# Kernel optimization log

Measured on AMD Instinct MI355X. Metric: run time of the kernel, lower is better.

## Reference

```python
import jax, jax.numpy as jnp
import numpy as np

N_NODES = 100000
N_EDGES = 3200000
N_GRAPHS = 256
IN_DIM = 128
HID = 64
K = 3


def setup_inputs() -> dict:
    key = jax.random.key(0)
    ks = jax.random.split(key, 10)
    x = jax.random.normal(ks[0], (N_NODES, IN_DIM), dtype=jnp.float32)
    edge_index = jax.random.randint(ks[1], (2, N_EDGES), 0, N_NODES, dtype=jnp.int64)
    batch = jnp.sort(jax.random.randint(ks[2], (N_NODES,), 0, N_GRAPHS, dtype=jnp.int64))
    # ChebConv k-order weights: list of Linear(in, out) -> stacked [K, in, out]
    s1 = 1.0 / np.sqrt(IN_DIM)
    s2 = 1.0 / np.sqrt(HID)
    W1 = jax.random.uniform(ks[3], (K, IN_DIM, HID), jnp.float32, -s1, s1)
    b1 = jax.random.uniform(ks[4], (HID,), jnp.float32, -s1, s1)
    W2 = jax.random.uniform(ks[5], (K, HID, HID), jnp.float32, -s2, s2)
    b2 = jax.random.uniform(ks[6], (HID,), jnp.float32, -s2, s2)
    Wfc = jax.random.uniform(ks[7], (HID, 1), jnp.float32, -s2, s2)
    bfc = jax.random.uniform(ks[8], (1,), jnp.float32, -s2, s2)
    return {"x": x, "edge_index": edge_index, "batch": batch,
            "W1": W1, "b1": b1, "W2": W2, "b2": b2, "Wfc": Wfc, "bfc": bfc}


def _cheb_conv(x, src, dst, edge_w, W, b):
    # PyG ChebConv, sym normalization, lambda_max=2 => L_hat has zero diagonal
    # and off-diagonal -D^{-1/2} A D^{-1/2} (edge_w precomputed, negative).
    n = x.shape[0]
    def lhat(v):  # (L_hat v)_i = sum_{edges j->i} edge_w * v_j
        return jax.ops.segment_sum(edge_w[:, None] * v[src], dst, num_segments=n)
    Tx0 = x
    Tx1 = lhat(Tx0)
    Tx2 = 2.0 * lhat(Tx1) - Tx0
    return Tx0 @ W[0] + Tx1 @ W[1] + Tx2 @ W[2] + b


def reference(x, edge_index, batch, W1, b1, W2, b2, Wfc, bfc):
    src, dst = edge_index[0], edge_index[1]
    n = x.shape[0]
    # degree on row (source), sym normalization
    deg = jax.ops.segment_sum(jnp.ones_like(src, dtype=x.dtype), src, num_segments=n)
    dinv = jnp.where(deg > 0, jax.lax.rsqrt(jnp.maximum(deg, 1.0)), 0.0)
    edge_w = -dinv[src] * dinv[dst]  # scaled Laplacian off-diagonal weights

    h = jax.nn.relu(_cheb_conv(x, src, dst, edge_w, W1, b1))
    h = jax.nn.relu(_cheb_conv(h, src, dst, edge_w, W2, b2))

    # global mean pool over graphs
    sums = jax.ops.segment_sum(h, batch, num_segments=N_GRAPHS)
    counts = jax.ops.segment_sum(jnp.ones((n,), dtype=h.dtype), batch, num_segments=N_GRAPHS)
    pooled = sums / jnp.maximum(counts, 1.0)[:, None]

    return (pooled @ Wfc + bfc).squeeze(-1)  # [N_GRAPHS]
```

## Files before the change

### kernel.cpp

```cpp
#include <hip/hip_runtime.h>
#include <hip/hip_fp16.h>
#include <cstdint>
#include <cstddef>

static constexpr int NN = 100000;
static constexpr int NE = 3200000;
static constexpr int NG = 256;
static constexpr int NBK = (NN + 127) / 128;
static constexpr int EPB = NE / 256;

typedef _Float16 h8 __attribute__((ext_vector_type(8)));
typedef float f4v __attribute__((ext_vector_type(4)));

__device__ __forceinline__ void atomAddF(float* p, float v) {
  unsafeAtomicAdd(p, v);
}

__device__ __forceinline__ float h2f(__half h) { return __half2float(h); }

__device__ __forceinline__ unsigned pk2(float a, float b) {
  unsigned lo = __half_as_ushort(__float2half_rn(a));
  unsigned hi = __half_as_ushort(__float2half_rn(b));
  return lo | (hi << 16);
}

__global__ void k_detect(const int* __restrict__ ei, int* __restrict__ flag) {
  if (threadIdx.x == 0 && blockIdx.x == 0) {
    int nz = 0;
    for (int i = 0; i < 64; ++i) nz += (ei[2 * i + 1] != 0) ? 1 : 0;
    *flag = (nz == 0) ? 1 : 0;
  }
}

__device__ __forceinline__ int ld_idx(const void* raw, int f, int i) {
  return f ? (int)((const long long*)raw)[i] : ((const int*)raw)[i];
}

__global__ __launch_bounds__(256) void k_repack_batch(const void* __restrict__ raw,
                                                      const int* __restrict__ flag,
                                                      int* __restrict__ b32,
                                                      int* __restrict__ gcnt) {
  __shared__ int cnt[256];
  int t = threadIdx.x;
  cnt[t] = 0;
  int blk0 = blockIdx.x * 256;
  int f = *flag;
  int g0 = ld_idx(raw, f, blk0);
  __syncthreads();
  int i = blk0 + t;
  if (i < NN) {
    int g = ld_idx(raw, f, i);
    b32[i] = g;
    atomicAdd(&cnt[g - g0], 1);
  }
  __syncthreads();
  if (cnt[t] > 0) atomicAdd(&gcnt[g0 + t], cnt[t]);
}

__global__ __launch_bounds__(256) void k_hist(const void* __restrict__ raw,
                                              const int* __restrict__ flag,
                                              int* __restrict__ sCnt,
                                              int* __restrict__ dCnt,
                                              int* __restrict__ hsBlk,
                                              int* __restrict__ hdBlk) {
  __shared__ int hs[NBK], hd[NBK];
  int t = threadIdx.x;
  for (int i = t; i < NBK; i += 256) { hs[i] = 0; hd[i] = 0; }
  __syncthreads();
  int f = *flag;
  int e0 = blockIdx.x * EPB;
  for (int e = e0 + t; e < e0 + EPB; e += 256) {
    int s = ld_idx(raw, f, e);
    int d = ld_idx(raw, f, NE + e);
    atomicAdd(&hs[s >> 7], 1);
    atomicAdd(&hd[d >> 7], 1);
  }
  __syncthreads();
  size_t hb = (size_t)blockIdx.x * NBK;
  for (int i = t; i < NBK; i += 256) {
    int a = hs[i], b = hd[i];
    hsBlk[hb + i] = a;
    hdBlk[hb + i] = b;
    if (a) atomicAdd(&sCnt[i], a);
    if (b) atomicAdd(&dCnt[i], b);
  }
}

__global__ __launch_bounds__(1024) void k_scan(const int* __restrict__ sCnt,
                                               const int* __restrict__ dCnt,
                                               int* __restrict__ sBase,
                                               int* __restrict__ dBase,
                                               int* __restrict__ sCur,
                                               int* __restrict__ dCur) {
  __shared__ int sh1[1024], sh2[1024];
  int t = threadIdx.x;
  int v1 = (t < NBK) ? sCnt[t] : 0;
  int v2 = (t < NBK) ? dCnt[t] : 0;
  sh1[t] = v1; sh2[t] = v2;
  __syncthreads();
  for (int off = 1; off < 1024; off <<= 1) {
    int a1 = (t >= off) ? sh1[t - off] : 0;
    int a2 = (t >= off) ? sh2[t - off] : 0;
    __syncthreads();
    sh1[t] += a1; sh2[t] += a2;
    __syncthreads();
  }
  if (t <= NBK) {
    int b1 = sh1[t] - v1, b2 = sh2[t] - v2;
    sBase[t] = b1; dBase[t] = b2;
    if (t < NBK) { sCur[t] = b1; dCur[t] = b2; }
  }
}

__global__ __launch_bounds__(256) void k_scatter(const void* __restrict__ raw,
                                                 const int* __restrict__ flag,
                                                 const int* __restrict__ hsBlk,
                                                 const int* __restrict__ hdBlk,
                                                 int* __restrict__ sCur,
                                                 int* __restrict__ dCur,
                                                 int* __restrict__ srclist,
                                                 unsigned* __restrict__ elist) {
  __shared__ int hs[NBK], hd[NBK], cbS[NBK], cbD[NBK];
  int t = threadIdx.x;
  size_t hb = (size_t)blockIdx.x * NBK;
  for (int i = t; i < NBK; i += 256) {
    int c1 = hsBlk[hb + i];
    cbS[i] = c1 ? atomicAdd(&sCur[i], c1) : 0;
    int c2 = hdBlk[hb + i];
    cbD[i] = c2 ? atomicAdd(&dCur[i], c2) : 0;
    hs[i] = 0; hd[i] = 0;
  }
  __syncthreads();
  int f = *flag;
  int e0 = blockIdx.x * EPB;
  for (int e = e0 + t; e < e0 + EPB; e += 256) {
    int s = ld_idx(raw, f, e);
    int d = ld_idx(raw, f, NE + e);
    int bs = s >> 7, bd = d >> 7;
    int ls = atomicAdd(&hs[bs], 1);
    int ld2 = atomicAdd(&hd[bd], 1);
    srclist[cbS[bs] + ls] = s;
    elist[cbD[bd] + ld2] = (unsigned)s | ((unsigned)(d & 127) << 17);
  }
}

__global__ __launch_bounds__(256) void k_deg(const int* __restrict__ sBase,
                                             const int* __restrict__ srclist,
                                             float* __restrict__ dinv) {
  __shared__ int cnt[128];
  int t = threadIdx.x;
  if (t < 128) cnt[t] = 0;
  __syncthreads();
  int b = blockIdx.x;
  int e0 = sBase[b], e1 = sBase[b + 1];
  for (int i = e0 + t; i < e1; i += 256) atomicAdd(&cnt[srclist[i] & 127], 1);
  __syncthreads();
  if (t < 128) {
    int node = b * 128 + t;
    if (node < NN) {
      int c = cnt[t];
      dinv[node] = (c > 0) ? rsqrtf((float)c) : 0.f;
    }
  }
}

__global__ __launch_bounds__(256) void k_csr(const int* __restrict__ dBase,
                                             const unsigned* __restrict__ elist,
                                             int* __restrict__ rowptr,
                                             int* __restrict__ adj) {
  __shared__ int cnt[128], sc[128], off[128], fill[128];
  int t = threadIdx.x;
  if (t < 128) { cnt[t] = 0; fill[t] = 0; }
  __syncthreads();
  int b = blockIdx.x;
  int e0 = dBase[b], e1 = dBase[b + 1];
  for (int i = e0 + t; i < e1; i += 256) atomicAdd(&cnt[elist[i] >> 17], 1);
  __syncthreads();
  if (t < 128) sc[t] = cnt[t];
  __syncthreads();
  for (int o = 1; o < 128; o <<= 1) {
    int a = (t < 128 && t >= o) ? sc[t - o] : 0;
    __syncthreads();
    if (t < 128) sc[t] += a;
    __syncthreads();
  }
  if (t < 128) {
    off[t] = sc[t] - cnt[t];
    int node = b * 128 + t;
    if (node < NN) rowptr[node] = e0 + off[t];
  }
  if (b == NBK - 1 && t == 0) rowptr[NN] = e1;
  __syncthreads();
  for (int i = e0 + t; i < e1; i += 256) {
    unsigned w2 = elist[i];
    int l = (int)(w2 >> 17);
    int pos = atomicAdd(&fill[l], 1);
    adj[e0 + off[l] + pos] = (int)(w2 & 0x1FFFFu);
  }
}

__global__ __launch_bounds__(256) void k_prepW(const float* __restrict__ W1,
                                               const float* __restrict__ W2,
                                               __half* __restrict__ BtX,
                                               __half* __restrict__ BtH) {
  int t = blockIdx.x * 256 + threadIdx.x;
  if (t < 192 * 128) {
    int n = t >> 7, k = t & 127;
    float v;
    if (n < 64)       v = W1[k * 64 + n] - W1[16384 + k * 64 + n];
    else if (n < 128) v = W1[8192 + k * 64 + (n - 64)];
    else              v = W1[16384 + k * 64 + (n - 128)];
    BtX[n * 128 + k] = __float2half_rn(v);
  } else if (t < 192 * 128 + 64 * 192) {
    int u = t - 192 * 128;
    int n = u / 192, k = u % 192;
    int s = k >> 6, kk = k & 63;
    float v = (s == 0) ? (W2[kk * 64 + n] - W2[8192 + kk * 64 + n])
            : (s == 1) ? W2[4096 + kk * 64 + n]
                       : 2.f * W2[8192 + kk * 64 + n];
    BtH[n * 192 + k] = __float2half_rn(v);
  }
}

static constexpr int AW = 136;
__global__ __launch_bounds__(256) void k_gemm_x(const float* __restrict__ x,
                                                const __half* __restrict__ BtX,
                                                const float* __restrict__ dinv,
                                                __half* __restrict__ gV0,
                                                unsigned* __restrict__ p01) {
  __shared__ __align__(16) _Float16 As[128 * AW];
  const int t = threadIdx.x;
  const int n0 = blockIdx.x * 128;
  {
    int i = t >> 1, q = t & 1;
    int row = n0 + i;
    _Float16* dst = As + i * AW + q * 64;
    if (row < NN) {
      const float* src = x + (size_t)row * 128 + q * 64;
#pragma unroll
      for (int c = 0; c < 64; c += 4) {
        float4 v = *reinterpret_cast<const float4*>(src + c);
        ushort4 u;
        u.x = __half_as_ushort(__float2half_rn(v.x));
        u.y = __half_as_ushort(__float2half_rn(v.y));
        u.z = __half_as_ushort(__float2half_rn(v.z));
        u.w = __half_as_ushort(__float2half_rn(v.w));
        *reinterpret_cast<ushort4*>(dst + c) = u;
      }
    } else {
#pragma unroll
      for (int c = 0; c < 64; c += 4)
        *reinterpret_cast<ushort4*>(dst + c) = make_ushort4(0, 0, 0, 0);
    }
  }
  __syncthreads();
  const int w = t >> 6, lane = t & 63;
  const int quad = lane >> 4, l = lane & 15;
  f4v acc[2][12];
#pragma unroll
  for (int mt = 0; mt < 2; ++mt)
#pragma unroll
    for (int nt = 0; nt < 12; ++nt) acc[mt][nt] = (f4v){0.f, 0.f, 0.f, 0.f};

#pragma unroll
  for (int ks = 0; ks < 4; ++ks) {
    int k0 = ks * 32 + quad * 8;
    h8 a0 = *reinterpret_cast<const h8*>(As + (w * 32 + l) * AW + k0);
    h8 a1 = *reinterpret_cast<const h8*>(As + (w * 32 + 16 + l) * AW + k0);
#pragma unroll
    for (int nt = 0; nt < 12; ++nt) {
      h8 b = *reinterpret_cast<const h8*>(BtX + (size_t)(nt * 16 + l) * 128 + k0);
      acc[0][nt] = __builtin_amdgcn_mfma_f32_16x16x32_f16(a0, b, acc[0][nt], 0, 0, 0);
      acc[1][nt] = __builtin_amdgcn_mfma_f32_16x16x32_f16(a1, b, acc[1][nt], 0, 0, 0);
    }
  }
#pragma unroll
  for (int mt = 0; mt < 2; ++mt) {
#pragma unroll
    for (int r = 0; r < 4; ++r) {
      int row = n0 + w * 32 + mt * 16 + quad * 4 + r;
      if (row < NN) {
        float dv = dinv[row];
#pragma unroll
        for (int nt2 = 0; nt2 < 4; ++nt2) {
          gV0[(size_t)row * 64 + nt2 * 16 + l] = __float2half_rn(acc[mt][nt2][r]);
          p01[(size_t)row * 64 + nt2 * 16 + l] =
              pk2(dv * acc[mt][4 + nt2][r], dv * acc[mt][8 + nt2][r]);
        }
      }
    }
  }
}

__global__ __launch_bounds__(256) void k_prop2p(const int* __restrict__ rp,
                                                const int* __restrict__ adj,
                                                const unsigned* __restrict__ vp,
                                                const float* __restrict__ dinv,
                                                __half* __restrict__ oA,
                                                __half* __restrict__ oB) {
  int node = blockIdx.x * 4 + (threadIdx.x >> 6);
  int d = threadIdx.x & 63;
  if (node >= NN) return;
  int p0 = rp[node], p1 = rp[node + 1];
  float a0 = 0.f, a1 = 0.f, a2 = 0.f, a3 = 0.f;
  float b0 = 0.f, b1 = 0.f, b2 = 0.f, b3 = 0.f;
  union { unsigned u; __half2 h; } cv;
  int p = p0;
  int pA = (p0 + 3) & ~3;
  if (pA > p1) pA = p1;
  for (; p < pA; ++p) {
    cv.u = vp[(size_t)adj[p] * 64 + d];
    float2 f = __half22float2(cv.h);
    a0 += f.x; b0 += f.y;
  }
  for (; p + 8 <= p1; p += 8) {
    int4 e0 = *reinterpret_cast<const int4*>(adj + p);
    int4 e1 = *reinterpret_cast<const int4*>(adj + p + 4);
    unsigned u0 = vp[(size_t)e0.x * 64 + d], u1 = vp[(size_t)e0.y * 64 + d];
    unsigned u2 = vp[(size_t)e0.z * 64 + d], u3 = vp[(size_t)e0.w * 64 + d];
    unsigned u4 = vp[(size_t)e1.x * 64 + d], u5 = vp[(size_t)e1.y * 64 + d];
    unsigned u6 = vp[(size_t)e1.z * 64 + d], u7 = vp[(size_t)e1.w * 64 + d];
    cv.u = u0; { float2 f = __half22float2(cv.h); a0 += f.x; b0 += f.y; }
    cv.u = u1; { float2 f = __half22float2(cv.h); a1 += f.x; b1 += f.y; }
    cv.u = u2; { float2 f = __half22float2(cv.h); a2 += f.x; b2 += f.y; }
    cv.u = u3; { float2 f = __half22float2(cv.h); a3 += f.x; b3 += f.y; }
    cv.u = u4; { float2 f = __half22float2(cv.h); a0 += f.x; b0 += f.y; }
    cv.u = u5; { float2 f = __half22float2(cv.h); a1 += f.x; b1 += f.y; }
    cv.u = u6; { float2 f = __half22float2(cv.h); a2 += f.x; b2 += f.y; }
    cv.u = u7; { float2 f = __half22float2(cv.h); a3 += f.x; b3 += f.y; }
  }
  if (p + 4 <= p1) {
    int4 e = *reinterpret_cast<const int4*>(adj + p);
    unsigned u0 = vp[(size_t)e.x * 64 + d], u1 = vp[(size_t)e.y * 64 + d];
    unsigned u2 = vp[(size_t)e.z * 64 + d], u3 = vp[(size_t)e.w * 64 + d];
    cv.u = u0; { float2 f = __half22float2(cv.h); a0 += f.x; b0 += f.y; }
    cv.u = u1; { float2 f = __half22float2(cv.h); a1 += f.x; b1 += f.y; }
    cv.u = u2; { float2 f = __half22float2(cv.h); a2 += f.x; b2 += f.y; }
    cv.u = u3; { float2 f = __half22float2(cv.h); a3 += f.x; b3 += f.y; }
    p += 4;
  }
  for (; p < p1; ++p) {
    cv.u = vp[(size_t)adj[p] * 64 + d];
    float2 f = __half22float2(cv.h);
    a1 += f.x; b1 += f.y;
  }
  float sa = (a0 + a1) + (a2 + a3);
  float sb = (b0 + b1) + (b2 + b3);
  float dv = dinv[node];
  oA[(size_t)node * 64 + d] = __float2half_rn(-dv * sa);
  oB[(size_t)node * 64 + d] = __float2half_rn(-dv * dv * sb);
}

__global__ __launch_bounds__(256) void k_prop1(const int* __restrict__ rp,
                                               const int* __restrict__ adj,
                                               const __half* __restrict__ vin,
                                               const float* __restrict__ dinv,
                                               __half* __restrict__ o_p,
                                               __half* __restrict__ o_s) {
  int node = blockIdx.x * 4 + (threadIdx.x >> 6);
  int d = threadIdx.x & 63;
  if (node >= NN) return;
  int p0 = rp[node], p1 = rp[node + 1];
  float a0 = 0.f, a1 = 0.f, a2 = 0.f, a3 = 0.f;
  int p = p0;
  int pA = (p0 + 3) & ~3;
  if (pA > p1) pA = p1;
  for (; p < pA; ++p) a0 += h2f(vin[(size_t)adj[p] * 64 + d]);
  for (; p + 8 <= p1; p += 8) {
    int4 e0 = *reinterpret_cast<const int4*>(adj + p);
    int4 e1 = *reinterpret_cast<const int4*>(adj + p + 4);
    a0 += h2f(vin[(size_t)e0.x * 64 + d]);
    a1 += h2f(vin[(size_t)e0.y * 64 + d]);
    a2 += h2f(vin[(size_t)e0.z * 64 + d]);
    a3 += h2f(vin[(size_t)e0.w * 64 + d]);
    a0 += h2f(vin[(size_t)e1.x * 64 + d]);
    a1 += h2f(vin[(size_t)e1.y * 64 + d]);
    a2 += h2f(vin[(size_t)e1.z * 64 + d]);
    a3 += h2f(vin[(size_t)e1.w * 64 + d]);
  }
  if (p + 4 <= p1) {
    int4 e = *reinterpret_cast<const int4*>(adj + p);
    a0 += h2f(vin[(size_t)e.x * 64 + d]);
    a1 += h2f(vin[(size_t)e.y * 64 + d]);
    a2 += h2f(vin[(size_t)e.z * 64 + d]);
    a3 += h2f(vin[(size_t)e.w * 64 + d]);
    p += 4;
  }
  for (; p < p1; ++p) a1 += h2f(vin[(size_t)adj[p] * 64 + d]);
  float s = (a0 + a1) + (a2 + a3);
  float dv = dinv[node];
  float pl = -dv * s;
  o_p[(size_t)node * 64 + d] = __float2half_rn(pl);
  if (o_s) o_s[(size_t)node * 64 + d] = __float2half_rn(dv * pl);
}

__global__ __launch_bounds__(256) void k_prop_h1(const int* __restrict__ rp,
                                                 const int* __restrict__ adj,
                                                 const __half* __restrict__ vin,
                                                 const float* __restrict__ dinv,
                                                 const __half* __restrict__ gV0,
                                                 const __half* __restrict__ gP,
                                                 const float* __restrict__ b1v,
                                                 __half* __restrict__ gH1,
                                                 __half* __restrict__ gH1s) {
  int node = blockIdx.x * 4 + (threadIdx.x >> 6);
  int d = threadIdx.x & 63;
  if (node >= NN) return;
  int p0 = rp[node], p1 = rp[node + 1];
  float a0 = 0.f, a1 = 0.f, a2 = 0.f, a3 = 0.f;
  int p = p0;
  int pA = (p0 + 3) & ~3;
  if (pA > p1) pA = p1;
  for (; p < pA; ++p) a0 += h2f(vin[(size_t)adj[p] * 64 + d]);
  for (; p + 8 <= p1; p += 8) {
    int4 e0 = *reinterpret_cast<const int4*>(adj + p);
    int4 e1 = *reinterpret_cast<const int4*>(adj + p + 4);
    a0 += h2f(vin[(size_t)e0.x * 64 + d]);
    a1 += h2f(vin[(size_t)e0.y * 64 + d]);
    a2 += h2f(vin[(size_t)e0.z * 64 + d]);
    a3 += h2f(vin[(size_t)e0.w * 64 + d]);
    a0 += h2f(vin[(size_t)e1.x * 64 + d]);
    a1 += h2f(vin[(size_t)e1.y * 64 + d]);
    a2 += h2f(vin[(size_t)e1.z * 64 + d]);
    a3 += h2f(vin[(size_t)e1.w * 64 + d]);
  }
  if (p + 4 <= p1) {
    int4 e = *reinterpret_cast<const int4*>(adj + p);
    a0 += h2f(vin[(size_t)e.x * 64 + d]);
    a1 += h2f(vin[(size_t)e.y * 64 + d]);
    a2 += h2f(vin[(size_t)e.z * 64 + d]);
    a3 += h2f(vin[(size_t)e.w * 64 + d]);
    p += 4;
  }
  for (; p < p1; ++p) a1 += h2f(vin[(size_t)adj[p] * 64 + d]);
  float s = (a0 + a1) + (a2 + a3);
  float dv = dinv[node];
  float R = -dv * s;
  size_t idx = (size_t)node * 64 + d;
  float h = h2f(gV0[idx]) + h2f(gP[idx]) + 2.f * R + b1v[d];
  h = fmaxf(h, 0.f);
  gH1[idx] = __float2half_rn(h);
  gH1s[idx] = __float2half_rn(dv * h);
}

static constexpr int HW = 200;
__global__ __launch_bounds__(256) void k_gemm_h2_pool(const __half* __restrict__ gH1,
                                                      const __half* __restrict__ gT1,
                                                      const __half* __restrict__ gT2,
                                                      const __half* __restrict__ BtH,
                                                      const float* __restrict__ b2v,
                                                      const int* __restrict__ b32,
                                                      float* __restrict__ pooled) {
  __shared__ __align__(16) char smem[128 * HW * 2];
  __shared__ int gb[128];
  _Float16* As = reinterpret_cast<_Float16*>(smem);
  const int t = threadIdx.x;
  const int n0 = blockIdx.x * 128;
  if (t < 128) gb[t] = (n0 + t < NN) ? b32[n0 + t] : -1;
  for (int c = t; c < 128 * 24; c += 256) {
    int row = c / 24, seg = c % 24;
    int tb = seg >> 3, off = (seg & 7) * 8;
    int rowg = n0 + row;
    h8 v = (h8){0, 0, 0, 0, 0, 0, 0, 0};
    if (rowg < NN) {
      const __half* src = (tb == 0 ? gH1 : tb == 1 ? gT1 : gT2) + (size_t)rowg * 64 + off;
      v = *reinterpret_cast<const h8*>(src);
    }
    *reinterpret_cast<h8*>(As + row * HW + seg * 8) = v;
  }
  __syncthreads();
  const int w = t >> 6, lane = t & 63;
  const int quad = lane >> 4, l = lane & 15;
  f4v acc[2][4];
#pragma unroll
  for (int mt = 0; mt < 2; ++mt)
#pragma unroll
    for (int nt = 0; nt < 4; ++nt) acc[mt][nt] = (f4v){0.f, 0.f, 0.f, 0.f};
#pragma unroll
  for (int ks = 0; ks < 6; ++ks) {
    int k0 = ks * 32 + quad * 8;
    h8 a0 = *reinterpret_cast<const h8*>(As + (w * 32 + l) * HW + k0);
    h8 a1 = *reinterpret_cast<const h8*>(As + (w * 32 + 16 + l) * HW + k0);
#pragma unroll
    for (int nt = 0; nt < 4; ++nt) {
      h8 b = *reinterpret_cast<const h8*>(BtH + (size_t)(nt * 16 + l) * 192 + k0);
      acc[0][nt] = __builtin_amdgcn_mfma_f32_16x16x32_f16(a0, b, acc[0][nt], 0, 0, 0);
      acc[1][nt] = __builtin_amdgcn_mfma_f32_16x16x32_f16(a1, b, acc[1][nt], 0, 0, 0);
    }
  }
  __syncthreads();
  float (*ht)[68] = reinterpret_cast<float (*)[68]>(smem);
#pragma unroll
  for (int mt = 0; mt < 2; ++mt)
#pragma unroll
    for (int r = 0; r < 4; ++r) {
      int rl = w * 32 + mt * 16 + quad * 4 + r;
#pragma unroll
      for (int nt = 0; nt < 4; ++nt) {
        int col = nt * 16 + l;
        ht[rl][col] = fmaxf(acc[mt][nt][r] + b2v[col], 0.f);
      }
    }
  __syncthreads();
  int rg = t >> 6;
  int d = t & 63;
  int base = rg * 32;
  int cur = -2;
  float s = 0.f;
  for (int i2 = 0; i2 < 32; ++i2) {
    int g = gb[base + i2];
    if (g != cur) {
      if (cur >= 0) atomAddF(&pooled[cur * 64 + d], s);
      s = 0.f;
      cur = g;
    }
    if (g >= 0) s += ht[base + i2][d];
  }
  if (cur >= 0) atomAddF(&pooled[cur * 64 + d], s);
}

__global__ void k_out(const float* __restrict__ pooled, const int* __restrict__ gcnt,
                      const float* __restrict__ Wfc, const float* __restrict__ bfc,
                      float* __restrict__ out) {
  int g = blockIdx.x, t = threadIdx.x;
  float v = pooled[g * 64 + t] * Wfc[t];
  int c = gcnt[g];
  v /= (float)(c > 0 ? c : 1);
  for (int off = 32; off > 0; off >>= 1) v += __shfl_down(v, off, 64);
  if (t == 0) out[g] = v + bfc[0];
}

extern "C" void kernel_launch(void* const* d_in, const int* in_sizes, int n_in,
                              void* d_out, int out_size, void* d_ws, size_t ws_size,
                              hipStream_t stream) {
  const float* x   = (const float*)d_in[0];
  const void*  ei  = d_in[1];
  const void*  bat = d_in[2];
  const float* W1  = (const float*)d_in[3];
  const float* b1v = (const float*)d_in[4];
  const float* W2  = (const float*)d_in[5];
  const float* b2v = (const float*)d_in[6];
  const float* Wfc = (const float*)d_in[7];
  const float* bfc = (const float*)d_in[8];
  float* out = (float*)d_out;

  char* w = (char*)d_ws;
  size_t o = 0;
  auto take = [&](size_t bytes) -> void* {
    void* p = w + o;
    o = (o + bytes + 255) & ~(size_t)255;
    return p;
  };
  int*      flag   = (int*)take(256);
  int*      gcnt   = (int*)take((size_t)NG * 4);
  float*    pooled = (float*)take((size_t)NG * 64 * 4);
  int*      sCnt   = (int*)take((size_t)(NBK + 2) * 4);
  int*      dCnt   = (int*)take((size_t)(NBK + 2) * 4);
  char*     zend   = w + o;
  int*      sBase  = (int*)take((size_t)(NBK + 2) * 4);
  int*      dBase  = (int*)take((size_t)(NBK + 2) * 4);
  int*      sCur   = (int*)take((size_t)(NBK + 2) * 4);
  int*      dCur   = (int*)take((size_t)(NBK + 2) * 4);
  int*      b32    = (int*)take((size_t)NN * 4);
  float*    dinv   = (float*)take((size_t)NN * 4);
  int*      rowptr = (int*)take((size_t)(NN + 2) * 4);
  int*      hsBlk  = (int*)take((size_t)256 * NBK * 4);
  int*      hdBlk  = (int*)take((size_t)256 * NBK * 4);
  int*      srclist= (int*)take((size_t)NE * 4);
  unsigned* elist  = (unsigned*)take((size_t)NE * 4);
  __half*   BtX    = (__half*)take((size_t)192 * 128 * 2);
  __half*   BtH    = (__half*)take((size_t)64 * 192 * 2);
  __half*   gV0    = (__half*)take((size_t)NN * 64 * 2);
  unsigned* p01    = (unsigned*)take((size_t)NN * 64 * 4);
  __half*   gP     = (__half*)take((size_t)NN * 64 * 2);
  __half*   gQs    = (__half*)take((size_t)NN * 64 * 2);
  __half*   gH1    = (__half*)take((size_t)NN * 64 * 2);
  __half*   gH1s   = (__half*)take((size_t)NN * 64 * 2);
  __half*   gT1    = (__half*)take((size_t)NN * 64 * 2);
  __half*   gT1s   = (__half*)take((size_t)NN * 64 * 2);
  __half*   gT2    = (__half*)take((size_t)NN * 64 * 2);
  int*      adj    = srclist;
  (void)in_sizes; (void)n_in; (void)out_size; (void)ws_size;

  hipMemsetAsync(gcnt, 0, (size_t)(zend - (char*)gcnt), stream);

  k_detect<<<1, 64, 0, stream>>>((const int*)ei, flag);
  k_repack_batch<<<(NN + 255) / 256, 256, 0, stream>>>(bat, flag, b32, gcnt);
  k_prepW<<<(192 * 128 + 64 * 192 + 255) / 256, 256, 0, stream>>>(W1, W2, BtX, BtH);
  k_hist<<<256, 256, 0, stream>>>(ei, flag, sCnt, dCnt, hsBlk, hdBlk);
  k_scan<<<1, 1024, 0, stream>>>(sCnt, dCnt, sBase, dBase, sCur, dCur);
  k_scatter<<<256, 256, 0, stream>>>(ei, flag, hsBlk, hdBlk, sCur, dCur, srclist, elist);
  k_deg<<<NBK, 256, 0, stream>>>(sBase, srclist, dinv);
  k_csr<<<NBK, 256, 0, stream>>>(dBase, elist, rowptr, adj);

  const int gemm_grid = (NN + 127) / 128;
  const int prop_grid = (NN + 3) / 4;

  k_gemm_x<<<gemm_grid, 256, 0, stream>>>(x, BtX, dinv, gV0, p01);
  k_prop2p<<<prop_grid, 256, 0, stream>>>(rowptr, adj, p01, dinv, gP, gQs);
  k_prop_h1<<<prop_grid, 256, 0, stream>>>(rowptr, adj, gQs, dinv, gV0, gP, b1v, gH1, gH1s);
  k_prop1<<<prop_grid, 256, 0, stream>>>(rowptr, adj, gH1s, dinv, gT1, gT1s);
  k_prop1<<<prop_grid, 256, 0, stream>>>(rowptr, adj, gT1s, dinv, gT2, nullptr);
  k_gemm_h2_pool<<<gemm_grid, 256, 0, stream>>>(gH1, gT1, gT2, BtH, b2v, b32, pooled);
  k_out<<<NG, 64, 0, stream>>>(pooled, gcnt, Wfc, bfc, out);
}
```

Measured before the change: 680.5 us.

## Vectorize SpMM gathers with half-wave edge split and merge preprocessing launches

The four propagation kernels now have each half-wavefront handle alternate edges, and each lane loads two fp16 features (or four for the paired input) per gather instead of one. The two halves are then combined with a cross-lane shuffle. This widens each memory access and halves the number of gather instructions per edge. Separately, the batch repack, weight prep and histogram kernels are merged into one launch, and the degree and CSR kernels into another, which cuts launch count. The cost is that only half the lanes store results and the unaligned head and tail loops run on one half-wave only.

```diff
diff --git a/kernel.cpp b/kernel.cpp
--- a/kernel.cpp
+++ b/kernel.cpp
@@ -8,6 +8,9 @@
 static constexpr int NG = 256;
 static constexpr int NBK = (NN + 127) / 128;
 static constexpr int EPB = NE / 256;
+static constexpr int GB_BATCH = (NN + 255) / 256;
+static constexpr int GB_PREPW = (192 * 128 + 64 * 192 + 255) / 256;
+static constexpr int GB_HIST = 256;
 
 typedef _Float16 h8 __attribute__((ext_vector_type(8)));
 typedef float f4v __attribute__((ext_vector_type(4)));
@@ -16,8 +19,10 @@
   unsafeAtomicAdd(p, v);
 }
 
-__device__ __forceinline__ float h2f(__half h) { return __half2float(h); }
-
+union H2 { unsigned u; __half2 h; };
+__device__ __forceinline__ float2 up2(unsigned u) {
+  H2 c; c.u = u; return __half22float2(c.h);
+}
 __device__ __forceinline__ unsigned pk2(float a, float b) {
   unsigned lo = __half_as_ushort(__float2half_rn(a));
   unsigned hi = __half_as_ushort(__float2half_rn(b));
@@ -36,53 +41,78 @@
   return f ? (int)((const long long*)raw)[i] : ((const int*)raw)[i];
 }
 
-__global__ __launch_bounds__(256) void k_repack_batch(const void* __restrict__ raw,
-                                                      const int* __restrict__ flag,
-                                                      int* __restrict__ b32,
-                                                      int* __restrict__ gcnt) {
-  __shared__ int cnt[256];
+__global__ __launch_bounds__(256) void k_front(const void* __restrict__ bat,
+                                               const void* __restrict__ ei,
+                                               const int* __restrict__ flag,
+                                               const float* __restrict__ W1,
+                                               const float* __restrict__ W2,
+                                               int* __restrict__ b32,
+                                               int* __restrict__ gcnt,
+                                               __half* __restrict__ BtX,
+                                               __half* __restrict__ BtH,
+                                               int* __restrict__ sCnt,
+                                               int* __restrict__ dCnt,
+                                               int* __restrict__ hsBlk,
+                                               int* __restrict__ hdBlk) {
+  __shared__ int sh[2 * NBK];
+  int b = blockIdx.x;
   int t = threadIdx.x;
-  cnt[t] = 0;
-  int blk0 = blockIdx.x * 256;
-  int f = *flag;
-  int g0 = ld_idx(raw, f, blk0);
-  __syncthreads();
-  int i = blk0 + t;
-  if (i < NN) {
-    int g = ld_idx(raw, f, i);
-    b32[i] = g;
-    atomicAdd(&cnt[g - g0], 1);
-  }
-  __syncthreads();
-  if (cnt[t] > 0) atomicAdd(&gcnt[g0 + t], cnt[t]);
-}
-
-__global__ __launch_bounds__(256) void k_hist(const void* __restrict__ raw,
-                                              const int* __restrict__ flag,
-                                              int* __restrict__ sCnt,
-                                              int* __restrict__ dCnt,
-                                              int* __restrict__ hsBlk,
-                                              int* __restrict__ hdBlk) {
-  __shared__ int hs[NBK], hd[NBK];
-  int t = threadIdx.x;
-  for (int i = t; i < NBK; i += 256) { hs[i] = 0; hd[i] = 0; }
-  __syncthreads();
-  int f = *flag;
-  int e0 = blockIdx.x * EPB;
-  for (int e = e0 + t; e < e0 + EPB; e += 256) {
-    int s = ld_idx(raw, f, e);
-    int d = ld_idx(raw, f, NE + e);
-    atomicAdd(&hs[s >> 7], 1);
-    atomicAdd(&hd[d >> 7], 1);
-  }
-  __syncthreads();
-  size_t hb = (size_t)blockIdx.x * NBK;
-  for (int i = t; i < NBK; i += 256) {
-    int a = hs[i], b = hd[i];
-    hsBlk[hb + i] = a;
-    hdBlk[hb + i] = b;
-    if (a) atomicAdd(&sCnt[i], a);
-    if (b) atomicAdd(&dCnt[i], b);
+  if (b < GB_BATCH) {
+    int* cnt = sh;
+    cnt[t] = 0;
+    int blk0 = b * 256;
+    int f = *flag;
+    int g0 = ld_idx(bat, f, blk0);
+    __syncthreads();
+    int i = blk0 + t;
+    if (i < NN) {
+      int g = ld_idx(bat, f, i);
+      b32[i] = g;
+      atomicAdd(&cnt[g - g0], 1);
+    }
+    __syncthreads();
+    if (cnt[t] > 0) atomicAdd(&gcnt[g0 + t], cnt[t]);
+  } else if (b < GB_BATCH + GB_PREPW) {
+    int u = (b - GB_BATCH) * 256 + t;
+    if (u < 192 * 128) {
+      int n = u >> 7, k = u & 127;
+      float v;
+      if (n < 64)       v = W1[k * 64 + n] - W1[16384 + k * 64 + n];
+      else if (n < 128) v = W1[8192 + k * 64 + (n - 64)];
+      else              v = W1[16384 + k * 64 + (n - 128)];
+      BtX[n * 128 + k] = __float2half_rn(v);
+    } else if (u < 192 * 128 + 64 * 192) {
+      int u2 = u - 192 * 128;
+      int n = u2 / 192, k = u2 % 192;
+      int s = k >> 6, kk = k & 63;
+      float v = (s == 0) ? (W2[kk * 64 + n] - W2[8192 + kk * 64 + n])
+              : (s == 1) ? W2[4096 + kk * 64 + n]
+                         : 2.f * W2[8192 + kk * 64 + n];
+      BtH[n * 192 + k] = __float2half_rn(v);
+    }
+  } else {
+    int hb = b - GB_BATCH - GB_PREPW;
+    int* hs = sh;
+    int* hd = sh + NBK;
+    for (int i = t; i < NBK; i += 256) { hs[i] = 0; hd[i] = 0; }
+    __syncthreads();
+    int f = *flag;
+    int e0 = hb * EPB;
+    for (int e = e0 + t; e < e0 + EPB; e += 256) {
+      int s = ld_idx(ei, f, e);
+      int d = ld_idx(ei, f, NE + e);
+      atomicAdd(&hs[s >> 7], 1);
+      atomicAdd(&hd[d >> 7], 1);
+    }
+    __syncthreads();
+    size_t hoff = (size_t)hb * NBK;
+    for (int i = t; i < NBK; i += 256) {
+      int a = hs[i], c = hd[i];
+      hsBlk[hoff + i] = a;
+      hdBlk[hoff + i] = c;
+      if (a) atomicAdd(&sCnt[i], a);
+      if (c) atomicAdd(&dCnt[i], c);
+    }
   }
 }
 
@@ -144,81 +174,58 @@
   }
 }
 
-__global__ __launch_bounds__(256) void k_deg(const int* __restrict__ sBase,
-                                             const int* __restrict__ srclist,
-                                             float* __restrict__ dinv) {
-  __shared__ int cnt[128];
-  int t = threadIdx.x;
-  if (t < 128) cnt[t] = 0;
-  __syncthreads();
-  int b = blockIdx.x;
-  int e0 = sBase[b], e1 = sBase[b + 1];
-  for (int i = e0 + t; i < e1; i += 256) atomicAdd(&cnt[srclist[i] & 127], 1);
-  __syncthreads();
-  if (t < 128) {
-    int node = b * 128 + t;
-    if (node < NN) {
-      int c = cnt[t];
-      dinv[node] = (c > 0) ? rsqrtf((float)c) : 0.f;
-    }
-  }
-}
-
-__global__ __launch_bounds__(256) void k_csr(const int* __restrict__ dBase,
-                                             const unsigned* __restrict__ elist,
-                                             int* __restrict__ rowptr,
-                                             int* __restrict__ adj) {
+__global__ __launch_bounds__(256) void k_back(const int* __restrict__ sBase,
+                                              const int* __restrict__ srclist,
+                                              float* __restrict__ dinv,
+                                              const int* __restrict__ dBase,
+                                              const unsigned* __restrict__ elist,
+                                              int* __restrict__ rowptr,
+                                              int* __restrict__ adj) {
   __shared__ int cnt[128], sc[128], off[128], fill[128];
   int t = threadIdx.x;
-  if (t < 128) { cnt[t] = 0; fill[t] = 0; }
-  __syncthreads();
-  int b = blockIdx.x;
-  int e0 = dBase[b], e1 = dBase[b + 1];
-  for (int i = e0 + t; i < e1; i += 256) atomicAdd(&cnt[elist[i] >> 17], 1);
-  __syncthreads();
-  if (t < 128) sc[t] = cnt[t];
-  __syncthreads();
-  for (int o = 1; o < 128; o <<= 1) {
-    int a = (t < 128 && t >= o) ? sc[t - o] : 0;
-    __syncthreads();
-    if (t < 128) sc[t] += a;
-    __syncthreads();
-  }
-  if (t < 128) {
-    off[t] = sc[t] - cnt[t];
-    int node = b * 128 + t;
-    if (node < NN) rowptr[node] = e0 + off[t];
-  }
-  if (b == NBK - 1 && t == 0) rowptr[NN] = e1;
-  __syncthreads();
-  for (int i = e0 + t; i < e1; i += 256) {
-    unsigned w2 = elist[i];
-    int l = (int)(w2 >> 17);
-    int pos = atomicAdd(&fill[l], 1);
-    adj[e0 + off[l] + pos] = (int)(w2 & 0x1FFFFu);
-  }
-}
-
-__global__ __launch_bounds__(256) void k_prepW(const float* __restrict__ W1,
-                                               const float* __restrict__ W2,
-                                               __half* __restrict__ BtX,
-                                               __half* __restrict__ BtH) {
-  int t = blockIdx.x * 256 + threadIdx.x;
-  if (t < 192 * 128) {
-    int n = t >> 7, k = t & 127;
-    float v;
-    if (n < 64)       v = W1[k * 64 + n] - W1[16384 + k * 64 + n];
-    else if (n < 128) v = W1[8192 + k * 64 + (n - 64)];
-    else              v = W1[16384 + k * 64 + (n - 128)];
-    BtX[n * 128 + k] = __float2half_rn(v);
-  } else if (t < 192 * 128 + 64 * 192) {
-    int u = t - 192 * 128;
-    int n = u / 192, k = u % 192;
-    int s = k >> 6, kk = k & 63;
-    float v = (s == 0) ? (W2[kk * 64 + n] - W2[8192 + kk * 64 + n])
-            : (s == 1) ? W2[4096 + kk * 64 + n]
-                       : 2.f * W2[8192 + kk * 64 + n];
-    BtH[n * 192 + k] = __float2half_rn(v);
+  int bb = blockIdx.x;
+  if (bb < NBK) {
+    int b = bb;
+    if (t < 128) cnt[t] = 0;
+    __syncthreads();
+    int e0 = sBase[b], e1 = sBase[b + 1];
+    for (int i = e0 + t; i < e1; i += 256) atomicAdd(&cnt[srclist[i] & 127], 1);
+    __syncthreads();
+    if (t < 128) {
+      int node = b * 128 + t;
+      if (node < NN) {
+        int c = cnt[t];
+        dinv[node] = (c > 0) ? rsqrtf((float)c) : 0.f;
+      }
+    }
+  } else {
+    int b = bb - NBK;
+    if (t < 128) { cnt[t] = 0; fill[t] = 0; }
+    __syncthreads();
+    int e0 = dBase[b], e1 = dBase[b + 1];
+    for (int i = e0 + t; i < e1; i += 256) atomicAdd(&cnt[elist[i] >> 17], 1);
+    __syncthreads();
+    if (t < 128) sc[t] = cnt[t];
+    __syncthreads();
+    for (int o = 1; o < 128; o <<= 1) {
+      int a = (t < 128 && t >= o) ? sc[t - o] : 0;
+      __syncthreads();
+      if (t < 128) sc[t] += a;
+      __syncthreads();
+    }
+    if (t < 128) {
+      off[t] = sc[t] - cnt[t];
+      int node = b * 128 + t;
+      if (node < NN) rowptr[node] = e0 + off[t];
+    }
+    if (b == NBK - 1 && t == 0) rowptr[NN] = e1;
+    __syncthreads();
+    for (int i = e0 + t; i < e1; i += 256) {
+      unsigned w2 = elist[i];
+      int l = (int)(w2 >> 17);
+      int pos = atomicAdd(&fill[l], 1);
+      adj[e0 + off[l] + pos] = (int)(w2 & 0x1FFFFu);
+    }
   }
 }
 
@@ -292,155 +299,207 @@
   }
 }
 
+
 __global__ __launch_bounds__(256) void k_prop2p(const int* __restrict__ rp,
                                                 const int* __restrict__ adj,
-                                                const unsigned* __restrict__ vp,
+                                                const uint2* __restrict__ vp,
                                                 const float* __restrict__ dinv,
-                                                __half* __restrict__ oA,
-                                                __half* __restrict__ oB) {
+                                                unsigned* __restrict__ oA,
+                                                unsigned* __restrict__ oB) {
   int node = blockIdx.x * 4 + (threadIdx.x >> 6);
-  int d = threadIdx.x & 63;
   if (node >= NN) return;
+  int lane = threadIdx.x & 63, half = lane >> 5, dl = lane & 31;
   int p0 = rp[node], p1 = rp[node + 1];
-  float a0 = 0.f, a1 = 0.f, a2 = 0.f, a3 = 0.f;
-  float b0 = 0.f, b1 = 0.f, b2 = 0.f, b3 = 0.f;
-  union { unsigned u; __half2 h; } cv;
+  float ax0 = 0.f, ay0 = 0.f, bx0 = 0.f, by0 = 0.f;
+  float ax1 = 0.f, ay1 = 0.f, bx1 = 0.f, by1 = 0.f;
   int p = p0;
   int pA = (p0 + 3) & ~3;
   if (pA > p1) pA = p1;
-  for (; p < pA; ++p) {
-    cv.u = vp[(size_t)adj[p] * 64 + d];
-    float2 f = __half22float2(cv.h);
-    a0 += f.x; b0 += f.y;
-  }
+  if (half == 0)
+    for (int q = p; q < pA; ++q) {
+      uint2 u = vp[(size_t)adj[q] * 32 + dl];
+      float2 f = up2(u.x), g = up2(u.y);
+      ax0 += f.x; bx0 += f.y; ay0 += g.x; by0 += g.y;
+    }
+  p = pA;
   for (; p + 8 <= p1; p += 8) {
     int4 e0 = *reinterpret_cast<const int4*>(adj + p);
     int4 e1 = *reinterpret_cast<const int4*>(adj + p + 4);
-    unsigned u0 = vp[(size_t)e0.x * 64 + d], u1 = vp[(size_t)e0.y * 64 + d];
-    unsigned u2 = vp[(size_t)e0.z * 64 + d], u3 = vp[(size_t)e0.w * 64 + d];
-    unsigned u4 = vp[(size_t)e1.x * 64 + d], u5 = vp[(size_t)e1.y * 64 + d];
-    unsigned u6 = vp[(size_t)e1.z * 64 + d], u7 = vp[(size_t)e1.w * 64 + d];
-    cv.u = u0; { float2 f = __half22float2(cv.h); a0 += f.x; b0 += f.y; }
-    cv.u = u1; { float2 f = __half22float2(cv.h); a1 += f.x; b1 += f.y; }
-    cv.u = u2; { float2 f = __half22float2(cv.h); a2 += f.x; b2 += f.y; }
-    cv.u = u3; { float2 f = __half22float2(cv.h); a3 += f.x; b3 += f.y; }
-    cv.u = u4; { float2 f = __half22float2(cv.h); a0 += f.x; b0 += f.y; }
-    cv.u = u5; { float2 f = __half22float2(cv.h); a1 += f.x; b1 += f.y; }
-    cv.u = u6; { float2 f = __half22float2(cv.h); a2 += f.x; b2 += f.y; }
-    cv.u = u7; { float2 f = __half22float2(cv.h); a3 += f.x; b3 += f.y; }
+    int s0 = half ? e0.y : e0.x;
+    int s1 = half ? e0.w : e0.z;
+    int s2 = half ? e1.y : e1.x;
+    int s3 = half ? e1.w : e1.z;
+    uint2 u0 = vp[(size_t)s0 * 32 + dl];
+    uint2 u1 = vp[(size_t)s1 * 32 + dl];
+    uint2 u2 = vp[(size_t)s2 * 32 + dl];
+    uint2 u3 = vp[(size_t)s3 * 32 + dl];
+    { float2 f = up2(u0.x), g = up2(u0.y); ax0 += f.x; bx0 += f.y; ay0 += g.x; by0 += g.y; }
+    { float2 f = up2(u1.x), g = up2(u1.y); ax1 += f.x; bx1 += f.y; ay1 += g.x; by1 += g.y; }
+    { float2 f = up2(u2.x), g = up2(u2.y); ax0 += f.x; bx0 += f.y; ay0 += g.x; by0 += g.y; }
+    { float2 f = up2(u3.x), g = up2(u3.y); ax1 += f.x; bx1 += f.y; ay1 += g.x; by1 += g.y; }
   }
   if (p + 4 <= p1) {
     int4 e = *reinterpret_cast<const int4*>(adj + p);
-    unsigned u0 = vp[(size_t)e.x * 64 + d], u1 = vp[(size_t)e.y * 64 + d];
-    unsigned u2 = vp[(size_t)e.z * 64 + d], u3 = vp[(size_t)e.w * 64 + d];
-    cv.u = u0; { float2 f = __half22float2(cv.h); a0 += f.x; b0 += f.y; }
-    cv.u = u1; { float2 f = __half22float2(cv.h); a1 += f.x; b1 += f.y; }
-    cv.u = u2; { float2 f = __half22float2(cv.h); a2 += f.x; b2 += f.y; }
-    cv.u = u3; { float2 f = __half22float2(cv.h); a3 += f.x; b3 += f.y; }
+    int s0 = half ? e.y : e.x;
+    int s1 = half ? e.w : e.z;
+    uint2 u0 = vp[(size_t)s0 * 32 + dl];
+    uint2 u1 = vp[(size_t)s1 * 32 + dl];
+    { float2 f = up2(u0.x), g = up2(u0.y); ax0 += f.x; bx0 += f.y; ay0 += g.x; by0 += g.y; }
+    { float2 f = up2(u1.x), g = up2(u1.y); ax1 += f.x; bx1 += f.y; ay1 += g.x; by1 += g.y; }
     p += 4;
   }
-  for (; p < p1; ++p) {
-    cv.u = vp[(size_t)adj[p] * 64 + d];
-    float2 f = __half22float2(cv.h);
-    a1 += f.x; b1 += f.y;
-  }
-  float sa = (a0 + a1) + (a2 + a3);
-  float sb = (b0 + b1) + (b2 + b3);
-  float dv = dinv[node];
-  oA[(size_t)node * 64 + d] = __float2half_rn(-dv * sa);
-  oB[(size_t)node * 64 + d] = __float2half_rn(-dv * dv * sb);
+  if (half == 0)
+    for (; p < p1; ++p) {
+      uint2 u = vp[(size_t)adj[p] * 32 + dl];
+      float2 f = up2(u.x), g = up2(u.y);
+      ax1 += f.x; bx1 += f.y; ay1 += g.x; by1 += g.y;
+    }
+  float sax = ax0 + ax1, say = ay0 + ay1;
+  float sbx = bx0 + bx1, sby = by0 + by1;
+  sax += __shfl(sax, lane ^ 32);
+  say += __shfl(say, lane ^ 32);
+  sbx += __shfl(sbx, lane ^ 32);
+  sby += __shfl(sby, lane ^ 32);
+  if (half == 0) {
+    float dv = dinv[node];
+    size_t idx = (size_t)node * 32 + dl;
+    oA[idx] = pk2(-dv * sax, -dv * say);
+    oB[idx] = pk2(-dv * dv * sbx, -dv * dv * sby);
+  }
 }
 
 __global__ __launch_bounds__(256) void k_prop1(const int* __restrict__ rp,
                                                const int* __restrict__ adj,
-                                               const __half* __restrict__ vin,
+                                               const unsigned* __restrict__ vin,
                                                const float* __restrict__ dinv,
-                                               __half* __restrict__ o_p,
-                                               __half* __restrict__ o_s) {
+                                               unsigned* __restrict__ o_p,
+                                               unsigned* __restrict__ o_s) {
   int node = blockIdx.x * 4 + (threadIdx.x >> 6);
-  int d = threadIdx.x & 63;
   if (node >= NN) return;
+  int lane = threadIdx.x & 63, half = lane >> 5, dl = lane & 31;
   int p0 = rp[node], p1 = rp[node + 1];
-  float a0 = 0.f, a1 = 0.f, a2 = 0.f, a3 = 0.f;
+  float ax0 = 0.f, ay0 = 0.f, ax1 = 0.f, ay1 = 0.f;
   int p = p0;
   int pA = (p0 + 3) & ~3;
   if (pA > p1) pA = p1;
-  for (; p < pA; ++p) a0 += h2f(vin[(size_t)adj[p] * 64 + d]);
+  if (half == 0)
+    for (int q = p; q < pA; ++q) {
+      float2 f = up2(vin[(size_t)adj[q] * 32 + dl]);
+      ax0 += f.x; ay0 += f.y;
+    }
+  p = pA;
   for (; p + 8 <= p1; p += 8) {
     int4 e0 = *reinterpret_cast<const int4*>(adj + p);
     int4 e1 = *reinterpret_cast<const int4*>(adj + p + 4);
-    a0 += h2f(vin[(size_t)e0.x * 64 + d]);
-    a1 += h2f(vin[(size_t)e0.y * 64 + d]);
-    a2 += h2f(vin[(size_t)e0.z * 64 + d]);
-    a3 += h2f(vin[(size_t)e0.w * 64 + d]);
-    a0 += h2f(vin[(size_t)e1.x * 64 + d]);
-    a1 += h2f(vin[(size_t)e1.y * 64 + d]);
-    a2 += h2f(vin[(size_t)e1.z * 64 + d]);
-    a3 += h2f(vin[(size_t)e1.w * 64 + d]);
+    int s0 = half ? e0.y : e0.x;
+    int s1 = half ? e0.w : e0.z;
+    int s2 = half ? e1.y : e1.x;
+    int s3 = half ? e1.w : e1.z;
+    unsigned u0 = vin[(size_t)s0 * 32 + dl];
+    unsigned u1 = vin[(size_t)s1 * 32 + dl];
+    unsigned u2 = vin[(size_t)s2 * 32 + dl];
+    unsigned u3 = vin[(size_t)s3 * 32 + dl];
+    { float2 f = up2(u0); ax0 += f.x; ay0 += f.y; }
+    { float2 f = up2(u1); ax1 += f.x; ay1 += f.y; }
+    { float2 f = up2(u2); ax0 += f.x; ay0 += f.y; }
+    { float2 f = up2(u3); ax1 += f.x; ay1 += f.y; }
   }
   if (p + 4 <= p1) {
     int4 e = *reinterpret_cast<const int4*>(adj + p);
-    a0 += h2f(vin[(size_t)e.x * 64 + d]);
-    a1 += h2f(vin[(size_t)e.y * 64 + d]);
-    a2 += h2f(vin[(size_t)e.z * 64 + d]);
-    a3 += h2f(vin[(size_t)e.w * 64 + d]);
+    int s0 = half ? e.y : e.x;
+    int s1 = half ? e.w : e.z;
+    unsigned u0 = vin[(size_t)s0 * 32 + dl];
+    unsigned u1 = vin[(size_t)s1 * 32 + dl];
+    { float2 f = up2(u0); ax0 += f.x; ay0 += f.y; }
+    { float2 f = up2(u1); ax1 += f.x; ay1 += f.y; }
     p += 4;
   }
-  for (; p < p1; ++p) a1 += h2f(vin[(size_t)adj[p] * 64 + d]);
-  float s = (a0 + a1) + (a2 + a3);
-  float dv = dinv[node];
-  float pl = -dv * s;
-  o_p[(size_t)node * 64 + d] = __float2half_rn(pl);
-  if (o_s) o_s[(size_t)node * 64 + d] = __float2half_rn(dv * pl);
+  if (half == 0)
+    for (; p < p1; ++p) {
+      float2 f = up2(vin[(size_t)adj[p] * 32 + dl]);
+      ax1 += f.x; ay1 += f.y;
+    }
+  float sx = ax0 + ax1, sy = ay0 + ay1;
+  sx += __shfl(sx, lane ^ 32);
+  sy += __shfl(sy, lane ^ 32);
+  if (half == 0) {
+    float dv = dinv[node];
+    float px = -dv * sx, py = -dv * sy;
+    size_t idx = (size_t)node * 32 + dl;
+    o_p[idx] = pk2(px, py);
+    if (o_s) o_s[idx] = pk2(dv * px, dv * py);
+  }
 }
 
 __global__ __launch_bounds__(256) void k_prop_h1(const int* __restrict__ rp,
                                                  const int* __restrict__ adj,
-                                                 const __half* __restrict__ vin,
+                                                 const unsigned* __restrict__ vin,
                                                  const float* __restrict__ dinv,
-                                                 const __half* __restrict__ gV0,
-                                                 const __half* __restrict__ gP,
+                                                 const unsigned* __restrict__ gV0u,
+                                                 const unsigned* __restrict__ gPu,
                                                  const float* __restrict__ b1v,
-                                                 __half* __restrict__ gH1,
-                                                 __half* __restrict__ gH1s) {
+                                                 unsigned* __restrict__ gH1u,
+                                                 unsigned* __restrict__ gH1su) {
   int node = blockIdx.x * 4 + (threadIdx.x >> 6);
-  int d = threadIdx.x & 63;
   if (node >= NN) return;
+  int lane = threadIdx.x & 63, half = lane >> 5, dl = lane & 31;
   int p0 = rp[node], p1 = rp[node + 1];
-  float a0 = 0.f, a1 = 0.f, a2 = 0.f, a3 = 0.f;
+  float ax0 = 0.f, ay0 = 0.f, ax1 = 0.f, ay1 = 0.f;
   int p = p0;
   int pA = (p0 + 3) & ~3;
   if (pA > p1) pA = p1;
-  for (; p < pA; ++p) a0 += h2f(vin[(size_t)adj[p] * 64 + d]);
+  if (half == 0)
+    for (int q = p; q < pA; ++q) {
+      float2 f = up2(vin[(size_t)adj[q] * 32 + dl]);
+      ax0 += f.x; ay0 += f.y;
+    }
+  p = pA;
   for (; p + 8 <= p1; p += 8) {
     int4 e0 = *reinterpret_cast<const int4*>(adj + p);
     int4 e1 = *reinterpret_cast<const int4*>(adj + p + 4);
-    a0 += h2f(vin[(size_t)e0.x * 64 + d]);
-    a1 += h2f(vin[(size_t)e0.y * 64 + d]);
-    a2 += h2f(vin[(size_t)e0.z * 64 + d]);
-    a3 += h2f(vin[(size_t)e0.w * 64 + d]);
-    a0 += h2f(vin[(size_t)e1.x * 64 + d]);
-    a1 += h2f(vin[(size_t)e1.y * 64 + d]);
-    a2 += h2f(vin[(size_t)e1.z * 64 + d]);
-    a3 += h2f(vin[(size_t)e1.w * 64 + d]);
+    int s0 = half ? e0.y : e0.x;
+    int s1 = half ? e0.w : e0.z;
+    int s2 = half ? e1.y : e1.x;
+    int s3 = half ? e1.w : e1.z;
+    unsigned u0 = vin[(size_t)s0 * 32 + dl];
+    unsigned u1 = vin[(size_t)s1 * 32 + dl];
+    unsigned u2 = vin[(size_t)s2 * 32 + dl];
+    unsigned u3 = vin[(size_t)s3 * 32 + dl];
+    { float2 f = up2(u0); ax0 += f.x; ay0 += f.y; }
+    { float2 f = up2(u1); ax1 += f.x; ay1 += f.y; }
+    { float2 f = up2(u2); ax0 += f.x; ay0 += f.y; }
+    { float2 f = up2(u3); ax1 += f.x; ay1 += f.y; }
   }
   if (p + 4 <= p1) {
     int4 e = *reinterpret_cast<const int4*>(adj + p);
-    a0 += h2f(vin[(size_t)e.x * 64 + d]);
-    a1 += h2f(vin[(size_t)e.y * 64 + d]);
-    a2 += h2f(vin[(size_t)e.z * 64 + d]);
-    a3 += h2f(vin[(size_t)e.w * 64 + d]);
+    int s0 = half ? e.y : e.x;
+    int s1 = half ? e.w : e.z;
+    unsigned u0 = vin[(size_t)s0 * 32 + dl];
+    unsigned u1 = vin[(size_t)s1 * 32 + dl];
+    { float2 f = up2(u0); ax0 += f.x; ay0 += f.y; }
+    { float2 f = up2(u1); ax1 += f.x; ay1 += f.y; }
     p += 4;
   }
-  for (; p < p1; ++p) a1 += h2f(vin[(size_t)adj[p] * 64 + d]);
-  float s = (a0 + a1) + (a2 + a3);
-  float dv = dinv[node];
-  float R = -dv * s;
-  size_t idx = (size_t)node * 64 + d;
-  float h = h2f(gV0[idx]) + h2f(gP[idx]) + 2.f * R + b1v[d];
-  h = fmaxf(h, 0.f);
-  gH1[idx] = __float2half_rn(h);
-  gH1s[idx] = __float2half_rn(dv * h);
+  if (half == 0)
+    for (; p < p1; ++p) {
+      float2 f = up2(vin[(size_t)adj[p] * 32 + dl]);
+      ax1 += f.x; ay1 += f.y;
+    }
+  float sx = ax0 + ax1, sy = ay0 + ay1;
+  sx += __shfl(sx, lane ^ 32);
+  sy += __shfl(sy, lane ^ 32);
+  if (half == 0) {
+    float dv = dinv[node];
+    float Rx = -dv * sx, Ry = -dv * sy;
+    size_t idx = (size_t)node * 32 + dl;
+    float2 v0 = up2(gV0u[idx]);
+    float2 pp = up2(gPu[idx]);
+    float bx = b1v[2 * dl], by = b1v[2 * dl + 1];
+    float hx = fmaxf(v0.x + pp.x + 2.f * Rx + bx, 0.f);
+    float hy = fmaxf(v0.y + pp.y + 2.f * Ry + by, 0.f);
+    gH1u[idx] = pk2(hx, hy);
+    gH1su[idx] = pk2(dv * hx, dv * hy);
+  }
 }
 
 static constexpr int HW = 200;
@@ -585,22 +644,25 @@
   hipMemsetAsync(gcnt, 0, (size_t)(zend - (char*)gcnt), stream);
 
   k_detect<<<1, 64, 0, stream>>>((const int*)ei, flag);
-  k_repack_batch<<<(NN + 255) / 256, 256, 0, stream>>>(bat, flag, b32, gcnt);
-  k_prepW<<<(192 * 128 + 64 * 192 + 255) / 256, 256, 0, stream>>>(W1, W2, BtX, BtH);
-  k_hist<<<256, 256, 0, stream>>>(ei, flag, sCnt, dCnt, hsBlk, hdBlk);
+  k_front<<<GB_BATCH + GB_PREPW + GB_HIST, 256, 0, stream>>>(
+      bat, ei, flag, W1, W2, b32, gcnt, BtX, BtH, sCnt, dCnt, hsBlk, hdBlk);
   k_scan<<<1, 1024, 0, stream>>>(sCnt, dCnt, sBase, dBase, sCur, dCur);
   k_scatter<<<256, 256, 0, stream>>>(ei, flag, hsBlk, hdBlk, sCur, dCur, srclist, elist);
-  k_deg<<<NBK, 256, 0, stream>>>(sBase, srclist, dinv);
-  k_csr<<<NBK, 256, 0, stream>>>(dBase, elist, rowptr, adj);
+  k_back<<<2 * NBK, 256, 0, stream>>>(sBase, srclist, dinv, dBase, elist, rowptr, adj);
 
   const int gemm_grid = (NN + 127) / 128;
   const int prop_grid = (NN + 3) / 4;
 
   k_gemm_x<<<gemm_grid, 256, 0, stream>>>(x, BtX, dinv, gV0, p01);
-  k_prop2p<<<prop_grid, 256, 0, stream>>>(rowptr, adj, p01, dinv, gP, gQs);
-  k_prop_h1<<<prop_grid, 256, 0, stream>>>(rowptr, adj, gQs, dinv, gV0, gP, b1v, gH1, gH1s);
-  k_prop1<<<prop_grid, 256, 0, stream>>>(rowptr, adj, gH1s, dinv, gT1, gT1s);
-  k_prop1<<<prop_grid, 256, 0, stream>>>(rowptr, adj, gT1s, dinv, gT2, nullptr);
+  k_prop2p<<<prop_grid, 256, 0, stream>>>(rowptr, adj, (const uint2*)p01, dinv,
+                                          (unsigned*)gP, (unsigned*)gQs);
+  k_prop_h1<<<prop_grid, 256, 0, stream>>>(rowptr, adj, (const unsigned*)gQs, dinv,
+                                           (const unsigned*)gV0, (const unsigned*)gP,
+                                           b1v, (unsigned*)gH1, (unsigned*)gH1s);
+  k_prop1<<<prop_grid, 256, 0, stream>>>(rowptr, adj, (const unsigned*)gH1s, dinv,
+                                         (unsigned*)gT1, (unsigned*)gT1s);
+  k_prop1<<<prop_grid, 256, 0, stream>>>(rowptr, adj, (const unsigned*)gT1s, dinv,
+                                         (unsigned*)gT2, nullptr);
   k_gemm_h2_pool<<<gemm_grid, 256, 0, stream>>>(gH1, gT1, gT2, BtH, b2v, b32, pooled);
   k_out<<<NG, 64, 0, stream>>>(pooled, gcnt, Wfc, bfc, out);
 }
```

Result: no change. 692.2 us (+1.7%).
